# Kernel optimization log

Hardware: AMD Instinct MI355X
Metric: run time of the kernel (lower is better)

The kernel has to match this reference:

```python
import jax, jax.numpy as jnp
import numpy as np
from jax.scipy.special import logsumexp

DEG = 16        # neighbors per node (regular-degree graph)
EPS = 0.5       # entropic regularization
ALPHA = 0.5     # FGW structure/feature trade-off
N_OUTER = 5     # proximal (mirror-descent) outer iterations
N_SINK = 10     # Sinkhorn projection iterations per outer step


def setup_inputs() -> dict:
    key = jax.random.key(0)
    k1, k2, k3, k4 = jax.random.split(key, 4)
    N, d = 10000, 128
    T, K = 10, 10
    x = jax.random.normal(k1, (N, d), dtype=jnp.float32)
    # regular-degree COO edge_index: each node i receives DEG edges src -> i
    src = jax.random.randint(k2, (N * DEG,), 0, N, dtype=jnp.int32)
    dst = jnp.repeat(jnp.arange(N, dtype=jnp.int32), DEG)
    edge_index = jnp.stack([src, dst])  # [2, N*DEG]
    # template adjacency matrices (learned params), symmetric in [0,1]
    A = (jax.random.uniform(k3, (T, K, K)) < 0.4).astype(jnp.float32)
    templates = 0.5 * (A + jnp.swapaxes(A, 1, 2))
    templates_features = jax.random.normal(k4, (T, K, d), dtype=jnp.float32)
    return {"x": x, "edge_index": edge_index, "templates": templates,
            "templates_features": templates_features}


def _ltfgw(x, edge_index, templates, templates_features):
    N, d = x.shape
    T, K, _ = templates.shape
    m = DEG + 1
    # 1-hop neighborhood extraction: neighbors of node i are edge_index[0] rows
    # (regular degree -> rectangular gather, no ragged handling needed)
    src = edge_index[0].reshape(N, DEG)
    Fi = jnp.concatenate([x[:, None, :], x[src]], axis=1)  # [N, m, d]
    # local subgraph structure: star graph centered at the node
    Ci = jnp.zeros((m, m), x.dtype).at[0, 1:].set(1.0).at[1:, 0].set(1.0)
    p = jnp.full((m,), 1.0 / m, x.dtype)   # uniform weights on local nodes
    q = jnp.full((K,), 1.0 / K, x.dtype)   # uniform weights on template nodes
    logp, logq = jnp.log(p), jnp.log(q)

    def fgw(F_loc, Ft, Ct):
        # feature cost (mean sq. diff keeps magnitudes O(1))  [m, K]
        M = jnp.mean((F_loc[:, None, :] - Ft[None, :, :]) ** 2, axis=-1)
        constC = ((Ci ** 2) @ p)[:, None] + ((Ct ** 2) @ q)[None, :]

        def gw_tens(Tp):  # square-loss GW tensor product  [m, K]
            return constC - 2.0 * (Ci @ Tp @ Ct.T)

        def outer(logT, _):
            Tp = jnp.exp(logT)
            cost = (1.0 - ALPHA) * M + 2.0 * ALPHA * gw_tens(Tp)
            logKmat = logT - cost / EPS  # entropic mirror step (log-domain)

            def sink(c, _):
                f, g = c
                f = logp - logsumexp(logKmat + g[None, :], axis=1)
                g = logq - logsumexp(logKmat + f[:, None], axis=0)
                return (f, g), None

            (f, g), _ = jax.lax.scan(sink, (jnp.zeros_like(p), jnp.zeros_like(q)),
                                     None, length=N_SINK)
            return logKmat + f[:, None] + g[None, :], None

        logT0 = logp[:, None] + logq[None, :]
        logT, _ = jax.lax.scan(outer, logT0, None, length=N_OUTER)
        Tp = jnp.exp(logT)
        return jnp.sum(Tp * ((1.0 - ALPHA) * M + ALPHA * gw_tens(Tp)))

    per_tpl = jax.vmap(fgw, in_axes=(None, 0, 0))          # over templates
    return jax.vmap(per_tpl, in_axes=(0, None, None))(Fi, templates_features, templates)  # [N, T]


def reference(x, edge_index, templates, templates_features):
    return _ltfgw(x, edge_index, templates, templates_features)
```

## Files before the change

kernel.cpp:

```cpp
#include <hip/hip_runtime.h>

#define DEG 16
#define DD  128
#define KT  10
#define TT  10
#define MM  17
#define SLOTS 16
#define THREADS 256
#define EMS 11

#if __has_builtin(__builtin_amdgcn_exp2f)
#define FEXP2(x) __builtin_amdgcn_exp2f(x)
#else
#define FEXP2(x) exp2f(x)
#endif

#if __has_builtin(__builtin_amdgcn_rcpf)
#define FRCP(x) __builtin_amdgcn_rcpf(x)
#else
#define FRCP(x) (1.0f / (x))
#endif

#if __has_builtin(__builtin_amdgcn_logf)
#define FLOG2(x) __builtin_amdgcn_logf(x)
#else
#define FLOG2(x) __log2f(x)
#endif

#define TWO_LOG2E 2.8853900817779268f
#define NLOG2E    1.4426950408889634f
#define EPSLN2    0.34657359027997264f
#define RQP       0.5882352941176471f
#define VV0       0.5882352941176471f
#define PWQP      0.1f

typedef float v2f __attribute__((ext_vector_type(2)));
typedef float v4f __attribute__((ext_vector_type(4)));

__device__ __forceinline__ v2f pk_fma(v2f a, v2f b, v2f c) {
    asm("v_pk_fma_f32 %0, %1, %2, %0" : "+v"(c) : "v"(a), "v"(b));
    return c;
}
__device__ __forceinline__ v2f pk_fma_s(v2f a, v2f bs, v2f c) {
    asm("v_pk_fma_f32 %0, %1, %2, %0" : "+v"(c) : "v"(a), "s"(bs));
    return c;
}

template <int CTRL>
__device__ __forceinline__ float dpp_add(float x) {
    union { float f; int i; } a, b;
    a.f = x;
    b.i = __builtin_amdgcn_update_dpp(0, a.i, CTRL, 0xF, 0xF, true);
    return x + b.f;
}
__device__ __forceinline__ float sum16(float t) {
    t = dpp_add<0xB1>(t);
    t = dpp_add<0x4E>(t);
    t = dpp_add<0x124>(t);
    t = dpp_add<0x128>(t);
    return t;
}

#define _D(i, CTRL) "v_add_f32_dpp %" #i ", %" #i ", %" #i " " CTRL \
                    " row_mask:0xf bank_mask:0xf bound_ctrl:0\n\t"
#define _C1 "quad_perm:[1,0,3,2]"
#define _C2 "quad_perm:[2,3,0,1]"
#define _C3 "row_ror:4"
#define _C4 "row_ror:8"

__device__ __forceinline__ void sum16x5(float& a0, float& a1, float& a2,
                                        float& a3, float& a4) {
    asm("s_nop 1\n\t"
        _D(0,_C1) _D(1,_C1) _D(2,_C1) _D(3,_C1) _D(4,_C1)
        _D(0,_C2) _D(1,_C2) _D(2,_C2) _D(3,_C2) _D(4,_C2)
        _D(0,_C3) _D(1,_C3) _D(2,_C3) _D(3,_C3) _D(4,_C3)
        _D(0,_C4) _D(1,_C4) _D(2,_C4) _D(3,_C4) _D(4,_C4)
        : "+v"(a0), "+v"(a1), "+v"(a2), "+v"(a3), "+v"(a4));
}
__device__ __forceinline__ void sum16x6(float& a0, float& a1, float& a2,
                                        float& a3, float& a4, float& a5) {
    asm("s_nop 1\n\t"
        _D(0,_C1) _D(1,_C1) _D(2,_C1) _D(3,_C1) _D(4,_C1) _D(5,_C1)
        _D(0,_C2) _D(1,_C2) _D(2,_C2) _D(3,_C2) _D(4,_C2) _D(5,_C2)
        _D(0,_C3) _D(1,_C3) _D(2,_C3) _D(3,_C3) _D(4,_C3) _D(5,_C3)
        _D(0,_C4) _D(1,_C4) _D(2,_C4) _D(3,_C4) _D(4,_C4) _D(5,_C4)
        : "+v"(a0), "+v"(a1), "+v"(a2), "+v"(a3), "+v"(a4), "+v"(a5));
}
__device__ __forceinline__ void sumq3(float& a0, float& a1, float& a2) {
    asm("s_nop 1\n\t"
        _D(0,_C1) _D(1,_C1) _D(2,_C1)
        "s_nop 0\n\t"
        _D(0,_C2) _D(1,_C2) _D(2,_C2)
        : "+v"(a0), "+v"(a1), "+v"(a2));
}
__device__ __forceinline__ void sums5(float& a0, float& a1, float& a2,
                                      float& a3, float& a4) {
    asm("s_nop 1\n\t"
        _D(0,_C3) _D(1,_C3) _D(2,_C3) _D(3,_C3) _D(4,_C3)
        _D(0,_C4) _D(1,_C4) _D(2,_C4) _D(3,_C4) _D(4,_C4)
        : "+v"(a0), "+v"(a1), "+v"(a2), "+v"(a3), "+v"(a4));
}

__global__ __launch_bounds__(THREADS) void ltfgw_kernel(
    const float* __restrict__ x,
    const int*   __restrict__ ei,
    const float* __restrict__ tmpl,
    const float* __restrict__ tf,
    float* __restrict__ out,
    int N)
{
    __shared__ float sEM[SLOTS * MM * EMS];

    const int tid  = threadIdx.x;
    const int t    = blockIdx.y;
    const int slot = tid >> 4;
    const int lane = tid & 63;
    const int l    = lane & 15;
    const int gbase = lane & ~15;
    const int node  = blockIdx.x * SLOTS + slot;
    const int nodeC = (node < N) ? node : (N - 1);

    const int cl = (l < KT) ? l : 0;
    const float* ctp = tmpl + ((size_t)t * KT + cl) * KT;
    const float* tw  = tf + (size_t)t * KT * DD;

    float ct2q;
    {
        v2f r0 = *(const v2f*)(ctp);
        v2f r1 = *(const v2f*)(ctp + 2);
        v2f r2 = *(const v2f*)(ctp + 4);
        v2f r3 = *(const v2f*)(ctp + 6);
        v2f r4 = *(const v2f*)(ctp + 8);
        v2f acc = pk_fma(r0, r0, (v2f){0.f, 0.f});
        acc = pk_fma(r1, r1, acc);
        acc = pk_fma(r2, r2, acc);
        acc = pk_fma(r3, r3, acc);
        acc = pk_fma(r4, r4, acc);
        ct2q = (acc.x + acc.y) * (1.f / KT);
    }

    const int   srcl  = ei[nodeC * DEG + l];
    const float* myrow = x + (size_t)srcl * DD;
    v2f dotv[KT];
#pragma unroll
    for (int c = 0; c < KT; ++c) dotv[c] = (v2f){0.f, 0.f};
    v2f nrmv = (v2f){0.f, 0.f};
#pragma unroll 4
    for (int kk4 = 0; kk4 < 32; ++kk4) {
        v4f a4 = *(const v4f*)(myrow + kk4 * 4);
        nrmv = pk_fma(a4.lo, a4.lo, nrmv);
        nrmv = pk_fma(a4.hi, a4.hi, nrmv);
#pragma unroll
        for (int c = 0; c < KT; ++c) {
            v4f f4 = *(const v4f*)(tw + c * DD + kk4 * 4);
            dotv[c] = pk_fma_s(a4.lo, f4.lo, dotv[c]);
            dotv[c] = pk_fma_s(a4.hi, f4.hi, dotv[c]);
        }
    }
    float nrm_own = nrmv.x + nrmv.y;

    float dot0[KT], nft[KT], n0p;
    {
        const float* row0 = x + (size_t)nodeC * DD + 8 * l;
        v4f z0 = *(const v4f*)(row0);
        v4f z1 = *(const v4f*)(row0 + 4);
        v2f nn = pk_fma(z0.lo, z0.lo, (v2f){0.f, 0.f});
        nn = pk_fma(z0.hi, z0.hi, nn);
        nn = pk_fma(z1.lo, z1.lo, nn);
        nn = pk_fma(z1.hi, z1.hi, nn);
        n0p = nn.x + nn.y;
#pragma unroll
        for (int c = 0; c < KT; ++c) {
            const float* tr = tw + c * DD + 8 * l;
            v4f t0_ = *(const v4f*)(tr);
            v4f t1_ = *(const v4f*)(tr + 4);
            v2f d = pk_fma(z0.lo, t0_.lo, (v2f){0.f, 0.f});
            d = pk_fma(z0.hi, t0_.hi, d);
            d = pk_fma(z1.lo, t1_.lo, d);
            d = pk_fma(z1.hi, t1_.hi, d);
            dot0[c] = d.x + d.y;
            v2f nf = pk_fma(t0_.lo, t0_.lo, (v2f){0.f, 0.f});
            nf = pk_fma(t0_.hi, t0_.hi, nf);
            nf = pk_fma(t1_.lo, t1_.lo, nf);
            nf = pk_fma(t1_.hi, t1_.hi, nf);
            nft[c] = nf.x + nf.y;
        }
        sum16x6(dot0[0], dot0[1], dot0[2], dot0[3], dot0[4], dot0[5]);
        sum16x5(dot0[6], dot0[7], dot0[8], dot0[9], n0p);
        sum16x5(nft[0], nft[1], nft[2], nft[3], nft[4]);
        sum16x5(nft[5], nft[6], nft[7], nft[8], nft[9]);
    }

    const int obase = slot * (MM * EMS);
    {
        const int rb = obase + (l + 1) * EMS;
#pragma unroll
        for (int c = 0; c < KT; c += 2) {
            float eA = FEXP2(-NLOG2E * ((nrm_own + nft[c] - 2.f * (dotv[c].x + dotv[c].y)) * (1.f / DD)));
            float eB = FEXP2(-NLOG2E * ((nrm_own + nft[c + 1] - 2.f * (dotv[c + 1].x + dotv[c + 1].y)) * (1.f / DD)));
            *(v2f*)(&sEM[rb + c]) = (v2f){eA, eB};
        }
        if (l == 0) {
#pragma unroll
            for (int c = 0; c < KT; c += 2) {
                float eA = FEXP2(-NLOG2E * ((n0p + nft[c] - 2.f * dot0[c]) * (1.f / DD)));
                float eB = FEXP2(-NLOG2E * ((n0p + nft[c + 1] - 2.f * dot0[c + 1]) * (1.f / DD)));
                *(v2f*)(&sEM[obase + c]) = (v2f){eA, eB};
            }
        }
    }

    const int rg = l & 3, cg = l >> 2;
    const int cbase = 2 * cg + (cg < 2 ? cg : 2);
    const bool isd = (cg >= 2);
    const int c2o = isd ? 0 : 2;

    float Tp2[4][3], TK0l[3], vv[3];
#pragma unroll
    for (int i2 = 0; i2 < 4; ++i2) {
        Tp2[i2][0] = 1.f / (MM * KT);
        Tp2[i2][1] = 1.f / (MM * KT);
        Tp2[i2][2] = isd ? 0.f : (1.f / (MM * KT));
    }
    TK0l[0] = 1.f / (MM * KT);
    TK0l[1] = 1.f / (MM * KT);
    TK0l[2] = isd ? 0.f : (1.f / (MM * KT));
    float u2[4] = {0.f, 0.f, 0.f, 0.f}, u0_ = 0.f;
    float eK0u[3] = {0.f, 0.f, 0.f};

#pragma unroll 1
    for (int outer = 0; outer < 5; ++outer) {
        float s0 = ((Tp2[0][0] + Tp2[1][0]) + (Tp2[2][0] + Tp2[3][0]));
        float s1 = ((Tp2[0][1] + Tp2[1][1]) + (Tp2[2][1] + Tp2[3][1]));
        float s2 = ((Tp2[0][2] + Tp2[1][2]) + (Tp2[2][2] + Tp2[3][2]));
        sumq3(s0, s1, s2);
        s0 += TK0l[0]; s1 += TK0l[1]; s2 += TK0l[2];

        float sa0 = __shfl(s0, gbase + 0, 64),  ta0 = __shfl(TK0l[0], gbase + 0, 64);
        float sa1 = __shfl(s1, gbase + 0, 64),  ta1 = __shfl(TK0l[1], gbase + 0, 64);
        float sa2 = __shfl(s2, gbase + 0, 64),  ta2 = __shfl(TK0l[2], gbase + 0, 64);
        float sa3 = __shfl(s0, gbase + 4, 64),  ta3 = __shfl(TK0l[0], gbase + 4, 64);
        float sa4 = __shfl(s1, gbase + 4, 64),  ta4 = __shfl(TK0l[1], gbase + 4, 64);
        float sa5 = __shfl(s2, gbase + 4, 64),  ta5 = __shfl(TK0l[2], gbase + 4, 64);
        float sa6 = __shfl(s0, gbase + 8, 64),  ta6 = __shfl(TK0l[0], gbase + 8, 64);
        float sa7 = __shfl(s1, gbase + 8, 64),  ta7 = __shfl(TK0l[1], gbase + 8, 64);
        float sa8 = __shfl(s0, gbase + 12, 64), ta8 = __shfl(TK0l[0], gbase + 12, 64);
        float sa9 = __shfl(s1, gbase + 12, 64), ta9 = __shfl(TK0l[1], gbase + 12, 64);

        v2f r0 = *(const v2f*)(ctp);
        v2f r1 = *(const v2f*)(ctp + 2);
        v2f r2 = *(const v2f*)(ctp + 4);
        v2f r3 = *(const v2f*)(ctp + 6);
        v2f r4 = *(const v2f*)(ctp + 8);
        float Cs, C0;
        {
            float a = r0.x * sa0,   b = r0.y * sa1;
            a = fmaf(r1.x, sa2, a); b = fmaf(r1.y, sa3, b);
            a = fmaf(r2.x, sa4, a); b = fmaf(r2.y, sa5, b);
            a = fmaf(r3.x, sa6, a); b = fmaf(r3.y, sa7, b);
            a = fmaf(r4.x, sa8, a); b = fmaf(r4.y, sa9, b);
            Cs = a + b;
            float q = r0.x * ta0,   d = r0.y * ta1;
            q = fmaf(r1.x, ta2, q); d = fmaf(r1.y, ta3, d);
            q = fmaf(r2.x, ta4, q); d = fmaf(r2.y, ta5, d);
            q = fmaf(r3.x, ta6, q); d = fmaf(r3.y, ta7, d);
            q = fmaf(r4.x, ta8, q); d = fmaf(r4.y, ta9, d);
            C0 = q + d;
        }
        float e0 = FEXP2(-TWO_LOG2E * ((16.f / 17.f) + ct2q - 2.f * Cs));
        float e1 = FEXP2(-TWO_LOG2E * ((1.f  / 17.f) + ct2q - 2.f * C0));

        float E1_0 = __shfl(e1, gbase + cbase + 0, 64);
        float E1_1 = __shfl(e1, gbase + cbase + 1, 64);
        float E1_2 = __shfl(e1, gbase + cbase + 2, 64);
        float E0_0 = __shfl(e0, gbase + cbase + 0, 64);
        float E0_1 = __shfl(e0, gbase + cbase + 1, 64);
        float E0_2 = __shfl(e0, gbase + cbase + 2, 64);

#pragma unroll
        for (int i2 = 0; i2 < 4; ++i2) {
            const int jb = obase + (1 + rg + 4 * i2) * EMS + cbase;
            Tp2[i2][0] *= sEM[jb]       * E1_0;
            Tp2[i2][1] *= sEM[jb + 1]   * E1_1;
            Tp2[i2][2] *= sEM[jb + c2o] * E1_2;
        }
        eK0u[0] = TK0l[0] * (sEM[obase + cbase]       * E0_0);
        eK0u[1] = TK0l[1] * (sEM[obase + cbase + 1]   * E0_1);
        eK0u[2] = TK0l[2] * (sEM[obase + cbase + c2o] * E0_2);
        float eK0cc2 = isd ? 1.f : eK0u[2];
        vv[0] = VV0; vv[1] = VV0; vv[2] = VV0;

#pragma unroll 1
        for (int it = 0; it < 10; ++it) {
            float p0 = Tp2[0][0] * vv[0];
            p0 = fmaf(Tp2[0][1], vv[1], p0); p0 = fmaf(Tp2[0][2], vv[2], p0);
            float p1 = Tp2[1][0] * vv[0];
            p1 = fmaf(Tp2[1][1], vv[1], p1); p1 = fmaf(Tp2[1][2], vv[2], p1);
            float p2 = Tp2[2][0] * vv[0];
            p2 = fmaf(Tp2[2][1], vv[1], p2); p2 = fmaf(Tp2[2][2], vv[2], p2);
            float p3 = Tp2[3][0] * vv[0];
            p3 = fmaf(Tp2[3][1], vv[1], p3); p3 = fmaf(Tp2[3][2], vv[2], p3);
            float p4 = eK0u[0] * vv[0];
            p4 = fmaf(eK0u[1], vv[1], p4); p4 = fmaf(eK0u[2], vv[2], p4);
            sums5(p0, p1, p2, p3, p4);
            u2[0] = RQP * FRCP(p0);
            u2[1] = RQP * FRCP(p1);
            u2[2] = RQP * FRCP(p2);
            u2[3] = RQP * FRCP(p3);
            u0_   = RQP * FRCP(p4);
            float q0 = Tp2[0][0] * u2[0];
            q0 = fmaf(Tp2[1][0], u2[1], q0);
            q0 = fmaf(Tp2[2][0], u2[2], q0);
            q0 = fmaf(Tp2[3][0], u2[3], q0);
            float q1 = Tp2[0][1] * u2[0];
            q1 = fmaf(Tp2[1][1], u2[1], q1);
            q1 = fmaf(Tp2[2][1], u2[2], q1);
            q1 = fmaf(Tp2[3][1], u2[3], q1);
            float q2 = Tp2[0][2] * u2[0];
            q2 = fmaf(Tp2[1][2], u2[1], q2);
            q2 = fmaf(Tp2[2][2], u2[2], q2);
            q2 = fmaf(Tp2[3][2], u2[3], q2);
            sumq3(q0, q1, q2);
            vv[0] = FRCP(fmaf(eK0u[0], u0_, q0));
            vv[1] = FRCP(fmaf(eK0u[1], u0_, q1));
            vv[2] = FRCP(fmaf(eK0cc2, u0_, q2));
        }

        float puA = PWQP * u2[0], puB = PWQP * u2[1];
        float puC = PWQP * u2[2], puD = PWQP * u2[3];
        float pu0 = PWQP * u0_;
#pragma unroll
        for (int i = 0; i < 3; ++i) {
            Tp2[0][i] = (Tp2[0][i] * vv[i]) * puA;
            Tp2[1][i] = (Tp2[1][i] * vv[i]) * puB;
            Tp2[2][i] = (Tp2[2][i] * vv[i]) * puC;
            Tp2[3][i] = (Tp2[3][i] * vv[i]) * puD;
            TK0l[i]   = (eK0u[i]  * vv[i]) * pu0;
        }
    }

    {
        float s0 = ((Tp2[0][0] + Tp2[1][0]) + (Tp2[2][0] + Tp2[3][0]));
        float s1 = ((Tp2[0][1] + Tp2[1][1]) + (Tp2[2][1] + Tp2[3][1]));
        float s2 = ((Tp2[0][2] + Tp2[1][2]) + (Tp2[2][2] + Tp2[3][2]));
        sumq3(s0, s1, s2);
        s0 += TK0l[0]; s1 += TK0l[1]; s2 += TK0l[2];
        float sa0 = __shfl(s0, gbase + 0, 64),  ta0 = __shfl(TK0l[0], gbase + 0, 64);
        float sa1 = __shfl(s1, gbase + 0, 64),  ta1 = __shfl(TK0l[1], gbase + 0, 64);
        float sa2 = __shfl(s2, gbase + 0, 64),  ta2 = __shfl(TK0l[2], gbase + 0, 64);
        float sa3 = __shfl(s0, gbase + 4, 64),  ta3 = __shfl(TK0l[0], gbase + 4, 64);
        float sa4 = __shfl(s1, gbase + 4, 64),  ta4 = __shfl(TK0l[1], gbase + 4, 64);
        float sa5 = __shfl(s2, gbase + 4, 64),  ta5 = __shfl(TK0l[2], gbase + 4, 64);
        float sa6 = __shfl(s0, gbase + 8, 64),  ta6 = __shfl(TK0l[0], gbase + 8, 64);
        float sa7 = __shfl(s1, gbase + 8, 64),  ta7 = __shfl(TK0l[1], gbase + 8, 64);
        float sa8 = __shfl(s0, gbase + 12, 64), ta8 = __shfl(TK0l[0], gbase + 12, 64);
        float sa9 = __shfl(s1, gbase + 12, 64), ta9 = __shfl(TK0l[1], gbase + 12, 64);
        v2f r0 = *(const v2f*)(ctp);
        v2f r1 = *(const v2f*)(ctp + 2);
        v2f r2 = *(const v2f*)(ctp + 4);
        v2f r3 = *(const v2f*)(ctp + 6);
        v2f r4 = *(const v2f*)(ctp + 8);
        float Cs, C0;
        {
            float a = r0.x * sa0,   b = r0.y * sa1;
            a = fmaf(r1.x, sa2, a); b = fmaf(r1.y, sa3, b);
            a = fmaf(r2.x, sa4, a); b = fmaf(r2.y, sa5, b);
            a = fmaf(r3.x, sa6, a); b = fmaf(r3.y, sa7, b);
            a = fmaf(r4.x, sa8, a); b = fmaf(r4.y, sa9, b);
            Cs = a + b;
            float q = r0.x * ta0,   d = r0.y * ta1;
            q = fmaf(r1.x, ta2, q); d = fmaf(r1.y, ta3, d);
            q = fmaf(r2.x, ta4, q); d = fmaf(r2.y, ta5, d);
            q = fmaf(r3.x, ta6, q); d = fmaf(r3.y, ta7, d);
            q = fmaf(r4.x, ta8, q); d = fmaf(r4.y, ta9, d);
            C0 = q + d;
        }
        float g0l = (16.f / 17.f) + ct2q - 2.f * Cs;
        float g1l = (1.f  / 17.f) + ct2q - 2.f * C0;
        float G1_0 = __shfl(g1l, gbase + cbase + 0, 64);
        float G1_1 = __shfl(g1l, gbase + cbase + 1, 64);
        float G1_2 = __shfl(g1l, gbase + cbase + 2, 64);
        float G0_0 = __shfl(g0l, gbase + cbase + 0, 64);
        float G0_1 = __shfl(g0l, gbase + cbase + 1, 64);
        float G0_2 = __shfl(g0l, gbase + cbase + 2, 64);

        float objp = 0.f;
#pragma unroll
        for (int i2 = 0; i2 < 4; ++i2) {
            const int jb = obase + (1 + rg + 4 * i2) * EMS + cbase;
            objp += Tp2[i2][0] * (-EPSLN2 * FLOG2(sEM[jb])       + 0.5f * G1_0);
            objp += Tp2[i2][1] * (-EPSLN2 * FLOG2(sEM[jb + 1])   + 0.5f * G1_1);
            objp += Tp2[i2][2] * (-EPSLN2 * FLOG2(sEM[jb + c2o]) + 0.5f * G1_2);
        }
        float obj0p = TK0l[0] * (-EPSLN2 * FLOG2(sEM[obase + cbase])       + 0.5f * G0_0);
        obj0p      += TK0l[1] * (-EPSLN2 * FLOG2(sEM[obase + cbase + 1])   + 0.5f * G0_1);
        obj0p      += TK0l[2] * (-EPSLN2 * FLOG2(sEM[obase + cbase + c2o]) + 0.5f * G0_2);
        float tot = objp + ((rg == 0) ? obj0p : 0.f);
        float obj = sum16(tot);
        if (l == 0 && node < N) out[node * TT + t] = obj;
    }
}

extern "C" void kernel_launch(void* const* d_in, const int* in_sizes, int n_in,
                              void* d_out, int out_size, void* d_ws, size_t ws_size,
                              hipStream_t stream) {
    const float* x    = (const float*)d_in[0];
    const int*   ei   = (const int*)d_in[1];
    const float* tmpl = (const float*)d_in[2];
    const float* tf   = (const float*)d_in[3];
    float* out = (float*)d_out;
    int N = in_sizes[0] / DD;
    int gx = (N + SLOTS - 1) / SLOTS;
    hipLaunchKernelGGL(ltfgw_kernel, dim3(gx, TT), dim3(THREADS), 0, stream,
                       x, ei, tmpl, tf, out, N);
}
```

Before: 287.1 us.

## Remap blocks across XCDs for L2 reuse and drop redundant Sinkhorn scaling

Flattens the 2D grid into a 1D grid and remaps block indices so blocks on the same XCD process the same node groups for all templates. This aims to improve L2 hit rates on the gathered neighbor features. It also removes the constant scale factor from the Sinkhorn u updates and the initial v, which cancels in the transport plan, saving multiplies. Padding the grid to a multiple of 8 adds a few idle blocks.

```diff
diff --git a/kernel.cpp b/kernel.cpp
--- a/kernel.cpp
+++ b/kernel.cpp
@@ -30,8 +30,6 @@
 #define TWO_LOG2E 2.8853900817779268f
 #define NLOG2E    1.4426950408889634f
 #define EPSLN2    0.34657359027997264f
-#define RQP       0.5882352941176471f
-#define VV0       0.5882352941176471f
 #define PWQP      0.1f
 
 typedef float v2f __attribute__((ext_vector_type(2)));
@@ -112,12 +110,17 @@
     __shared__ float sEM[SLOTS * MM * EMS];
 
     const int tid  = threadIdx.x;
-    const int t    = blockIdx.y;
+    const int phys = blockIdx.x;
+    const int xcd  = phys & 7;
+    const int k    = phys >> 3;
+    const int t    = k % TT;
+    const int bx   = xcd + 8 * (k / TT);
+
     const int slot = tid >> 4;
     const int lane = tid & 63;
     const int l    = lane & 15;
     const int gbase = lane & ~15;
-    const int node  = blockIdx.x * SLOTS + slot;
+    const int node  = bx * SLOTS + slot;
     const int nodeC = (node < N) ? node : (N - 1);
 
     const int cl = (l < KT) ? l : 0;
@@ -215,7 +218,8 @@
     const bool isd = (cg >= 2);
     const int c2o = isd ? 0 : 2;
 
-    float Tp2[4][3], TK0l[3], vv[3];
+    float Tp2[4][3], TK0l[3];
+    float vv0, vv1, vv2;
 #pragma unroll
     for (int i2 = 0; i2 < 4; ++i2) {
         Tp2[i2][0] = 1.f / (MM * KT);
@@ -288,26 +292,26 @@
         eK0u[1] = TK0l[1] * (sEM[obase + cbase + 1]   * E0_1);
         eK0u[2] = TK0l[2] * (sEM[obase + cbase + c2o] * E0_2);
         float eK0cc2 = isd ? 1.f : eK0u[2];
-        vv[0] = VV0; vv[1] = VV0; vv[2] = VV0;
+        vv0 = 1.f; vv1 = 1.f; vv2 = 1.f;
 
 #pragma unroll 1
         for (int it = 0; it < 10; ++it) {
-            float p0 = Tp2[0][0] * vv[0];
-            p0 = fmaf(Tp2[0][1], vv[1], p0); p0 = fmaf(Tp2[0][2], vv[2], p0);
-            float p1 = Tp2[1][0] * vv[0];
-            p1 = fmaf(Tp2[1][1], vv[1], p1); p1 = fmaf(Tp2[1][2], vv[2], p1);
-            float p2 = Tp2[2][0] * vv[0];
-            p2 = fmaf(Tp2[2][1], vv[1], p2); p2 = fmaf(Tp2[2][2], vv[2], p2);
-            float p3 = Tp2[3][0] * vv[0];
-            p3 = fmaf(Tp2[3][1], vv[1], p3); p3 = fmaf(Tp2[3][2], vv[2], p3);
-            float p4 = eK0u[0] * vv[0];
-            p4 = fmaf(eK0u[1], vv[1], p4); p4 = fmaf(eK0u[2], vv[2], p4);
+            float p0 = Tp2[0][0] * vv0;
+            p0 = fmaf(Tp2[0][1], vv1, p0); p0 = fmaf(Tp2[0][2], vv2, p0);
+            float p1 = Tp2[1][0] * vv0;
+            p1 = fmaf(Tp2[1][1], vv1, p1); p1 = fmaf(Tp2[1][2], vv2, p1);
+            float p2 = Tp2[2][0] * vv0;
+            p2 = fmaf(Tp2[2][1], vv1, p2); p2 = fmaf(Tp2[2][2], vv2, p2);
+            float p3 = Tp2[3][0] * vv0;
+            p3 = fmaf(Tp2[3][1], vv1, p3); p3 = fmaf(Tp2[3][2], vv2, p3);
+            float p4 = eK0u[0] * vv0;
+            p4 = fmaf(eK0u[1], vv1, p4); p4 = fmaf(eK0u[2], vv2, p4);
             sums5(p0, p1, p2, p3, p4);
-            u2[0] = RQP * FRCP(p0);
-            u2[1] = RQP * FRCP(p1);
-            u2[2] = RQP * FRCP(p2);
-            u2[3] = RQP * FRCP(p3);
-            u0_   = RQP * FRCP(p4);
+            u2[0] = FRCP(p0);
+            u2[1] = FRCP(p1);
+            u2[2] = FRCP(p2);
+            u2[3] = FRCP(p3);
+            u0_   = FRCP(p4);
             float q0 = Tp2[0][0] * u2[0];
             q0 = fmaf(Tp2[1][0], u2[1], q0);
             q0 = fmaf(Tp2[2][0], u2[2], q0);
@@ -321,22 +325,29 @@
             q2 = fmaf(Tp2[2][2], u2[2], q2);
             q2 = fmaf(Tp2[3][2], u2[3], q2);
             sumq3(q0, q1, q2);
-            vv[0] = FRCP(fmaf(eK0u[0], u0_, q0));
-            vv[1] = FRCP(fmaf(eK0u[1], u0_, q1));
-            vv[2] = FRCP(fmaf(eK0cc2, u0_, q2));
+            vv0 = FRCP(fmaf(eK0u[0], u0_, q0));
+            vv1 = FRCP(fmaf(eK0u[1], u0_, q1));
+            vv2 = FRCP(fmaf(eK0cc2, u0_, q2));
         }
 
         float puA = PWQP * u2[0], puB = PWQP * u2[1];
         float puC = PWQP * u2[2], puD = PWQP * u2[3];
         float pu0 = PWQP * u0_;
-#pragma unroll
-        for (int i = 0; i < 3; ++i) {
-            Tp2[0][i] = (Tp2[0][i] * vv[i]) * puA;
-            Tp2[1][i] = (Tp2[1][i] * vv[i]) * puB;
-            Tp2[2][i] = (Tp2[2][i] * vv[i]) * puC;
-            Tp2[3][i] = (Tp2[3][i] * vv[i]) * puD;
-            TK0l[i]   = (eK0u[i]  * vv[i]) * pu0;
-        }
+        Tp2[0][0] = (Tp2[0][0] * vv0) * puA;
+        Tp2[0][1] = (Tp2[0][1] * vv1) * puA;
+        Tp2[0][2] = (Tp2[0][2] * vv2) * puA;
+        Tp2[1][0] = (Tp2[1][0] * vv0) * puB;
+        Tp2[1][1] = (Tp2[1][1] * vv1) * puB;
+        Tp2[1][2] = (Tp2[1][2] * vv2) * puB;
+        Tp2[2][0] = (Tp2[2][0] * vv0) * puC;
+        Tp2[2][1] = (Tp2[2][1] * vv1) * puC;
+        Tp2[2][2] = (Tp2[2][2] * vv2) * puC;
+        Tp2[3][0] = (Tp2[3][0] * vv0) * puD;
+        Tp2[3][1] = (Tp2[3][1] * vv1) * puD;
+        Tp2[3][2] = (Tp2[3][2] * vv2) * puD;
+        TK0l[0] = (eK0u[0] * vv0) * pu0;
+        TK0l[1] = (eK0u[1] * vv1) * pu0;
+        TK0l[2] = (eK0u[2] * vv2) * pu0;
     }
 
     {
@@ -410,7 +421,9 @@
     const float* tf   = (const float*)d_in[3];
     float* out = (float*)d_out;
     int N = in_sizes[0] / DD;
-    int gx = (N + SLOTS - 1) / SLOTS;
-    hipLaunchKernelGGL(ltfgw_kernel, dim3(gx, TT), dim3(THREADS), 0, stream,
+    int gxb = (N + SLOTS - 1) / SLOTS;
+    int mx  = (gxb + 7) / 8;
+    int grid = 8 * mx * TT;
+    hipLaunchKernelGGL(ltfgw_kernel, dim3(grid), dim3(THREADS), 0, stream,
                        x, ei, tmpl, tf, out, N);
 }
```

Result: faster. 279.9 us (-2.5%).
